# Performance work log

Measured on AMD Instinct MI355X. Metric: run time of the kernel, lower is better.

## Reference

```python
import jax, jax.numpy as jnp
import numpy as np

EPSILON = 0.1


def setup_inputs() -> dict:
    key = jax.random.key(0)
    ks = jax.random.split(key, 6)
    N, E, F_IN, F_OUT, NF = 50000, 800000, 256, 96, 3
    x = jax.random.normal(ks[0], (N, F_IN), dtype=jnp.float32)
    adj_vals = jax.random.uniform(ks[1], (E,), dtype=jnp.float32)
    d_scales = jax.random.uniform(ks[2], (NF, N), dtype=jnp.float32)
    # xavier-uniform-ish weights
    limit = np.sqrt(6.0 / (F_IN + F_OUT)).astype(np.float32)
    weights = jax.random.uniform(ks[3], (NF, F_IN, F_OUT), dtype=jnp.float32,
                                 minval=-limit, maxval=limit)
    bias = jnp.zeros((F_OUT,), dtype=jnp.float32)
    edge_index = jax.random.randint(ks[4], (2, E), 0, N, dtype=jnp.int32)
    return {"x": x, "adj_vals": adj_vals, "d_scales": d_scales,
            "weights": weights, "bias": bias, "edge_index": edge_index}


def reference(x, adj_vals, d_scales, weights, bias, edge_index):
    N = x.shape[0]
    row, col = edge_index[0], edge_index[1]

    # degree with self loops (add_remaining_self_loops adds 1 per node)
    deg = jax.ops.segment_sum(jnp.ones_like(adj_vals), row, num_segments=N) + 1.0
    eps_deg_inv = EPSILON / deg  # [N], diagonal of sparse_degree(..., epsilon)

    def spmm(t):  # symadj @ t via edge list
        return jax.ops.segment_sum(adj_vals[:, None] * t[col], row, num_segments=N)

    out = jnp.zeros((N, weights.shape[2]), dtype=x.dtype)
    n_filters = weights.shape[0]
    for ii in range(n_filters):
        sign = -1.0 if ii == 0 else 1.0  # Ad = symadj -/+ eps*diag(deg^-1)
        t = d_scales[ii][:, None] * (x @ weights[ii])          # D @ (x W)
        t = spmm(t) + sign * eps_deg_inv[:, None] * t          # Ad @ t
        t = d_scales[ii][:, None] * jax.nn.relu(t)             # D @ relu(t)
        out = out + t
    return out + bias
```

## Files before the change

kernel.cpp:

```cpp
#include <hip/hip_runtime.h>

#define EPSILON 0.1f
#define F_IN 256
#define F_OUT 96
#define NF 3
#define TCOLS 288
#define TSTRIDE 320
#define CAP 64
#define BN 96
#define CW 104
#define NCVT (TCOLS * F_IN / 4)

#define RPB 64
#define NBINS 782
#define BCAP 1536
#define EPB 4096

typedef __attribute__((ext_vector_type(8))) short bf8_t;
typedef __attribute__((ext_vector_type(4))) float f32x4;

__device__ inline ushort f2b(float f) {
    union { float f; unsigned u; } v; v.f = f;
    unsigned u = v.u;
    return (ushort)((u + 0x7FFFu + ((u >> 16) & 1u)) >> 16);
}
__device__ inline float blo(unsigned u) { return __uint_as_float(u << 16); }
__device__ inline float bhi(unsigned u) { return __uint_as_float(u & 0xffff0000u); }

__device__ inline bf8_t cvt8(float4 a, float4 b) {
    bf8_t r;
    r[0] = (short)f2b(a.x); r[1] = (short)f2b(a.y);
    r[2] = (short)f2b(a.z); r[3] = (short)f2b(a.w);
    r[4] = (short)f2b(b.x); r[5] = (short)f2b(b.y);
    r[6] = (short)f2b(b.z); r[7] = (short)f2b(b.w);
    return r;
}

__global__ __launch_bounds__(256) void setup_kernel(const float* __restrict__ w,
                                                    ushort* __restrict__ wt,
                                                    int* __restrict__ gcur) {
    int tid = blockIdx.x * 256 + threadIdx.x;
    if (tid < NCVT) {
        int base = tid * 4;
        int gc = base >> 8;
        int k  = base & 255;
        int ii = gc / F_OUT;
        int c  = gc - ii * F_OUT;
        const float* wp = w + (size_t)ii * (F_IN * F_OUT) + (size_t)k * F_OUT + c;
        ushort4 o;
        o.x = f2b(wp[0 * F_OUT]);
        o.y = f2b(wp[1 * F_OUT]);
        o.z = f2b(wp[2 * F_OUT]);
        o.w = f2b(wp[3 * F_OUT]);
        *(ushort4*)(wt + base) = o;
    } else {
        int z = (tid - NCVT) * 4;
        if (z + 3 < NBINS) {
            *(int4*)(gcur + z) = make_int4(0, 0, 0, 0);
        } else {
            for (int j = z; j < NBINS && j >= 0; ++j) gcur[j] = 0;
        }
    }
}

__global__ __launch_bounds__(256) void bin_cvt_kernel(
        const int* __restrict__ row, const int* __restrict__ col,
        const float* __restrict__ vals, int E,
        int* __restrict__ gcur, int2* __restrict__ gout,
        const float* __restrict__ x, ushort* __restrict__ xb, int N, int nbin) {
    __shared__ int2 ord[EPB];
    __shared__ int hist[NBINS];
    __shared__ int gbase[NBINS];
    __shared__ int basex[NBINS];
    __shared__ int ts[512];

    if ((int)blockIdx.x < nbin) {
        int tid = threadIdx.x;
        for (int i = tid; i < NBINS; i += 256) hist[i] = 0;
        __syncthreads();

        int e0 = (int)blockIdx.x * EPB;
        int4 r4[4], c4[4]; float4 v4[4];
        int rank[16], binv[16], valv[16];
        unsigned recx[16];
        #pragma unroll
        for (int g = 0; g < 4; ++g) {
            int e = e0 + tid * 4 + g * 1024;
            if (e + 3 < E) {
                r4[g] = *(const int4*)(row + e);
                c4[g] = *(const int4*)(col + e);
                v4[g] = *(const float4*)(vals + e);
            } else {
                int4 rr, cc; float4 vv;
                int* rp = (int*)&rr; int* cp = (int*)&cc; float* vp = (float*)&vv;
                #pragma unroll
                for (int j = 0; j < 4; ++j) {
                    int ee = e + j;
                    rp[j] = (ee < E) ? row[ee] : -1;
                    cp[j] = (ee < E) ? col[ee] : 0;
                    vp[j] = (ee < E) ? vals[ee] : 0.f;
                }
                r4[g] = rr; c4[g] = cc; v4[g] = vv;
            }
        }
        #pragma unroll
        for (int g = 0; g < 4; ++g) {
            const int* rp = (const int*)&r4[g];
            const int* cp = (const int*)&c4[g];
            const float* vp = (const float*)&v4[g];
            #pragma unroll
            for (int j = 0; j < 4; ++j) {
                int s = g * 4 + j;
                int r = rp[j];
                if (r >= 0) {
                    int b = r >> 6;
                    binv[s] = b;
                    recx[s] = (unsigned)(cp[j] & 0xffff) |
                              ((unsigned)(r & 63) << 16) | ((unsigned)b << 22);
                    valv[s] = __float_as_int(vp[j]);
                    rank[s] = atomicAdd(&hist[b], 1);
                } else {
                    binv[s] = -1; rank[s] = 0; recx[s] = 0; valv[s] = 0;
                }
            }
        }
        __syncthreads();

        int b0 = tid * 4;
        int h0 = (b0     < NBINS) ? hist[b0]     : 0;
        int h1 = (b0 + 1 < NBINS) ? hist[b0 + 1] : 0;
        int h2 = (b0 + 2 < NBINS) ? hist[b0 + 2] : 0;
        int h3 = (b0 + 3 < NBINS) ? hist[b0 + 3] : 0;
        int tot = h0 + h1 + h2 + h3;
        ts[tid] = tot;
        __syncthreads();
        int src = 0;
        #pragma unroll
        for (int off = 1; off < 256; off <<= 1) {
            int v = ts[src * 256 + tid];
            if (tid >= off) v += ts[src * 256 + tid - off];
            ts[(src ^ 1) * 256 + tid] = v;
            __syncthreads();
            src ^= 1;
        }
        int excl = ts[src * 256 + tid] - tot;
        if (b0     < NBINS) basex[b0]     = excl;
        if (b0 + 1 < NBINS) basex[b0 + 1] = excl + h0;
        if (b0 + 2 < NBINS) basex[b0 + 2] = excl + h0 + h1;
        if (b0 + 3 < NBINS) basex[b0 + 3] = excl + h0 + h1 + h2;
        #pragma unroll
        for (int q = 0; q < 4; ++q) {
            int i = b0 + q;
            if (i < NBINS) {
                int h = hist[i];
                gbase[i] = h ? atomicAdd(&gcur[i], h) : 0;
            }
        }
        __syncthreads();

        #pragma unroll
        for (int s = 0; s < 16; ++s)
            if (binv[s] >= 0)
                ord[basex[binv[s]] + rank[s]] = make_int2((int)recx[s], valv[s]);
        __syncthreads();

        int total = ts[src * 256 + 255];
        for (int i = tid; i < total; i += 256) {
            int2 rec = ord[i];
            int b = ((unsigned)rec.x) >> 22;
            int pos = gbase[b] + (i - basex[b]);
            if (pos < BCAP)
                gout[(size_t)b * BCAP + pos] = rec;
        }
    } else {
        size_t base = ((size_t)((int)blockIdx.x - nbin) * 256 + threadIdx.x) * 8;
        if (base < (size_t)N * F_IN) {
            float4 a = *(const float4*)(x + base);
            float4 b = *(const float4*)(x + base + 4);
            bf8_t o = cvt8(a, b);
            *(bf8_t*)(xb + base) = o;
        }
    }
}

__global__ __launch_bounds__(256) void bucket_kernel(
        const int2* __restrict__ gout, const int* __restrict__ gcur,
        int* __restrict__ cnt, int2* __restrict__ evs2, int N) {
    __shared__ int2 buck[RPB * CAP];
    __shared__ int lcnt[RPB];

    int tid = threadIdx.x;
    int b = blockIdx.x;
    if (tid < RPB) lcnt[tid] = 0;
    __syncthreads();

    int nrec = gcur[b];
    if (nrec > BCAP) nrec = BCAP;
    for (int i = tid; i < nrec; i += 256) {
        int2 rec = gout[(size_t)b * BCAP + i];
        int rl = (rec.x >> 16) & 63;
        int c  = rec.x & 0xffff;
        int k = atomicAdd(&lcnt[rl], 1);
        if (k < CAP) buck[rl * CAP + k] = make_int2(c, rec.y);
    }
    __syncthreads();

    int row0 = b * RPB;
    if (tid < RPB && row0 + tid < N) cnt[row0 + tid] = lcnt[tid];

    int lane = tid & 63, wave = tid >> 6;
    for (int r = wave; r < RPB; r += 4) {
        int rowg = row0 + r;
        if (rowg >= N) break;
        int m = min(lcnt[r], CAP);
        if (lane < m)
            evs2[(size_t)rowg * CAP + lane] = buck[r * CAP + lane];
    }
}

__global__ __launch_bounds__(256) void gemm_mfma(const ushort* __restrict__ xb,
                                                 const ushort* __restrict__ wt,
                                                 const float* __restrict__ dsc,
                                                 ushort* __restrict__ t, int N) {
    __shared__ ushort Bs[BN * F_IN];

    int tid = threadIdx.x;
    int lane = tid & 63, wave = tid >> 6;
    int cl = lane & 15, quad = lane >> 4;
    int mb = blockIdx.x / 3, cb = blockIdx.x - mb * 3;
    int gc0 = cb * BN;
    int m0 = mb * 64 + wave * 16;
    int mrow = m0 + cl;
    bool aok = (mrow < N);

    #pragma unroll
    for (int i = 0; i < 12; ++i) {
        int F = tid + i * 256;
        int rem = F & 63;
        int q = rem >> 4, c = rem & 15;
        int ksj = F >> 6;
        int ks = ksj / 6, j = ksj - ks * 6;
        int gc = gc0 + j * 16 + c;
        *(uint4*)(Bs + (size_t)F * 8) =
            *(const uint4*)(wt + (size_t)gc * F_IN + ks * 32 + q * 8);
    }

    uint4 areg[8];
    const ushort* xp = xb + (size_t)mrow * F_IN + quad * 8;
    const uint4 zu = make_uint4(0, 0, 0, 0);
    #pragma unroll
    for (int ks = 0; ks < 8; ++ks)
        areg[ks] = aok ? *(const uint4*)(xp + ks * 32) : zu;

    f32x4 acc[6];
    #pragma unroll
    for (int j = 0; j < 6; ++j) acc[j] = (f32x4){0.f, 0.f, 0.f, 0.f};

    __syncthreads();

    #pragma unroll
    for (int ks = 0; ks < 8; ++ks) {
        bf8_t a = *(const bf8_t*)&areg[ks];
        const ushort* bb = Bs + ((size_t)(ks * 6) * 64 + lane) * 8;
        #pragma unroll
        for (int j = 0; j < 6; ++j) {
            bf8_t b = *(const bf8_t*)(bb + j * 64 * 8);
            acc[j] = __builtin_amdgcn_mfma_f32_16x16x32_bf16(a, b, acc[j], 0, 0, 0);
        }
    }

    __syncthreads();
    ushort* Cw = Bs + wave * (16 * CW);
    float dscv[3][4];
    #pragma unroll
    for (int ii = 0; ii < 3; ++ii)
        #pragma unroll
        for (int r = 0; r < 4; ++r) {
            int rowg = m0 + quad * 4 + r;
            dscv[ii][r] = (rowg < N) ? dsc[(size_t)ii * N + rowg] : 0.f;
        }
    #pragma unroll
    for (int j = 0; j < 6; ++j) {
        int ii = (gc0 + j * 16) / F_OUT;
        #pragma unroll
        for (int r = 0; r < 4; ++r)
            Cw[(quad * 4 + r) * CW + j * 16 + cl] = f2b(dscv[ii][r] * acc[j][r]);
    }
    #pragma unroll
    for (int it = 0; it < 3; ++it) {
        int idx = lane + it * 64;
        int r = idx / 12, ch = idx - r * 12;
        int grow = m0 + r;
        if (grow < N)
            *(uint4*)(t + (size_t)grow * TSTRIDE + gc0 + ch * 8) =
                *(const uint4*)&Cw[r * CW + ch * 8];
    }
}

__device__ inline void acc8(float* acc, uint4 a, float v) {
    acc[0] = fmaf(v, blo(a.x), acc[0]); acc[1] = fmaf(v, bhi(a.x), acc[1]);
    acc[2] = fmaf(v, blo(a.y), acc[2]); acc[3] = fmaf(v, bhi(a.y), acc[3]);
    acc[4] = fmaf(v, blo(a.z), acc[4]); acc[5] = fmaf(v, bhi(a.z), acc[5]);
    acc[6] = fmaf(v, blo(a.w), acc[6]); acc[7] = fmaf(v, bhi(a.w), acc[7]);
}

__global__ __launch_bounds__(256) void spmm_kernel(const ushort* __restrict__ t,
                                                   const int2* __restrict__ evs2,
                                                   const int* __restrict__ cnt,
                                                   const float* __restrict__ dsc,
                                                   const float* __restrict__ bias,
                                                   float* __restrict__ out, int N) {
    int lane = threadIdx.x & 63;
    int wave = threadIdx.x >> 6;
    int n = blockIdx.x * 4 + wave;
    if (n >= N) return;

    int deg = cnt[n];
    int mm = (deg < CAP) ? deg : CAP;
    int s = n * CAP, e = s + mm;
    int coff = (lane < 40) ? lane * 8 : 0;

    float acc[8];
    #pragma unroll
    for (int j = 0; j < 8; ++j) acc[j] = 0.f;

    for (int base = s; base < e; base += 64) {
        int idx = base + lane;
        int2 q = make_int2(0, 0);
        if (idx < e) q = evs2[idx];
        int m = min(64, e - base);
        int j = 0;
        for (; j + 3 < m; j += 4) {
            int c0 = __shfl(q.x, j, 64);
            int c1 = __shfl(q.x, j + 1, 64);
            int c2 = __shfl(q.x, j + 2, 64);
            int c3 = __shfl(q.x, j + 3, 64);
            float v0 = __int_as_float(__shfl(q.y, j, 64));
            float v1 = __int_as_float(__shfl(q.y, j + 1, 64));
            float v2 = __int_as_float(__shfl(q.y, j + 2, 64));
            float v3 = __int_as_float(__shfl(q.y, j + 3, 64));
            uint4 a0 = *(const uint4*)(t + (size_t)c0 * TSTRIDE + coff);
            uint4 a1 = *(const uint4*)(t + (size_t)c1 * TSTRIDE + coff);
            uint4 a2 = *(const uint4*)(t + (size_t)c2 * TSTRIDE + coff);
            uint4 a3 = *(const uint4*)(t + (size_t)c3 * TSTRIDE + coff);
            acc8(acc, a0, v0);
            acc8(acc, a1, v1);
            acc8(acc, a2, v2);
            acc8(acc, a3, v3);
        }
        for (; j < m; ++j) {
            int c = __shfl(q.x, j, 64);
            float v = __int_as_float(__shfl(q.y, j, 64));
            uint4 a = *(const uint4*)(t + (size_t)c * TSTRIDE + coff);
            acc8(acc, a, v);
        }
    }

    float sign = (lane < 12) ? -1.f : 1.f;
    float epsdi = EPSILON / (float)(deg + 1);
    int ii = lane / 12;
    float dscv = (lane < 36) ? dsc[(size_t)ii * N + n] : 0.f;
    uint4 sv = *(const uint4*)(t + (size_t)n * TSTRIDE + coff);
    float se = sign * epsdi;
    float val[8];
    {
        unsigned u;
        u = sv.x; val[0] = fmaf(se, blo(u), acc[0]); val[1] = fmaf(se, bhi(u), acc[1]);
        u = sv.y; val[2] = fmaf(se, blo(u), acc[2]); val[3] = fmaf(se, bhi(u), acc[3]);
        u = sv.z; val[4] = fmaf(se, blo(u), acc[4]); val[5] = fmaf(se, bhi(u), acc[5]);
        u = sv.w; val[6] = fmaf(se, blo(u), acc[6]); val[7] = fmaf(se, bhi(u), acc[7]);
    }
    #pragma unroll
    for (int j = 0; j < 8; ++j) val[j] = fmaxf(val[j], 0.f) * dscv;

    float res[8];
    #pragma unroll
    for (int j = 0; j < 8; ++j) {
        float r1 = __shfl(val[j], lane + 12, 64);
        float r2 = __shfl(val[j], lane + 24, 64);
        res[j] = val[j] + r1 + r2;
    }
    if (lane < 12) {
        float4 b0 = *(const float4*)(bias + lane * 8);
        float4 b1 = *(const float4*)(bias + lane * 8 + 4);
        float4 o0 = make_float4(res[0] + b0.x, res[1] + b0.y, res[2] + b0.z, res[3] + b0.w);
        float4 o1 = make_float4(res[4] + b1.x, res[5] + b1.y, res[6] + b1.z, res[7] + b1.w);
        *(float4*)(out + (size_t)n * F_OUT + lane * 8) = o0;
        *(float4*)(out + (size_t)n * F_OUT + lane * 8 + 4) = o1;
    }
}

extern "C" void kernel_launch(void* const* d_in, const int* in_sizes, int n_in,
                              void* d_out, int out_size, void* d_ws, size_t ws_size,
                              hipStream_t stream) {
    const float* x    = (const float*)d_in[0];
    const float* adj  = (const float*)d_in[1];
    const float* dsc  = (const float*)d_in[2];
    const float* w    = (const float*)d_in[3];
    const float* bias = (const float*)d_in[4];
    const int*   ei   = (const int*)d_in[5];

    int E = in_sizes[1];
    int N = in_sizes[0] / F_IN;
    const int* row = ei;
    const int* col = ei + E;
    float* out = (float*)d_out;

    char* p = (char*)d_ws;
    auto take = [&](size_t bytes) {
        char* r = p;
        p += (bytes + 255) & ~(size_t)255;
        return r;
    };
    int*    cnt  = (int*)take((size_t)N * 4);
    int2*   evs2 = (int2*)take((size_t)N * CAP * 8);
    ushort* wt   = (ushort*)take((size_t)TCOLS * F_IN * 2);
    ushort* xb   = (ushort*)take((size_t)N * F_IN * 2);
    ushort* t    = (ushort*)take(((size_t)N * TSTRIDE + 256) * 2);
    int*    gcur = (int*)take((size_t)NBINS * 4);
    int2*   gout = (int2*)take((size_t)NBINS * BCAP * 8);

    int nzero = (NBINS + 3) / 4;
    setup_kernel<<<(NCVT + nzero + 255) / 256, 256, 0, stream>>>(w, wt, gcur);

    int nbin  = (E + EPB - 1) / EPB;
    int ncvtx = ((N * F_IN / 8) + 255) / 256;
    bin_cvt_kernel<<<nbin + ncvtx, 256, 0, stream>>>(row, col, adj, E, gcur, gout,
                                                     x, xb, N, nbin);
    bucket_kernel<<<NBINS, 256, 0, stream>>>(gout, gcur, cnt, evs2, N);
    gemm_mfma<<<3 * ((N + 63) / 64), 256, 0, stream>>>(xb, wt, dsc, t, N);
    spmm_kernel<<<(N + 3) / 4, 256, 0, stream>>>(t, evs2, cnt, dsc, bias, out, N);
}
```

Baseline: 231.5 us.

## Fuse bucket and GEMM kernels into one launch with XCD-aware tile mapping

```diff
diff --git a/kernel.cpp b/kernel.cpp
--- a/kernel.cpp
+++ b/kernel.cpp
@@ -183,59 +183,64 @@
     }
 }
 
-__global__ __launch_bounds__(256) void bucket_kernel(
+__global__ __launch_bounds__(512) void gemm_bucket(
+        const ushort* __restrict__ xb, const ushort* __restrict__ wt,
+        const float* __restrict__ dsc, ushort* __restrict__ t, int N,
+        int nper, int nw,
         const int2* __restrict__ gout, const int* __restrict__ gcur,
-        int* __restrict__ cnt, int2* __restrict__ evs2, int N) {
-    __shared__ int2 buck[RPB * CAP];
-    __shared__ int lcnt[RPB];
+        int* __restrict__ cnt, int2* __restrict__ evs2) {
+    __shared__ ushort Bs[BN * F_IN];
 
     int tid = threadIdx.x;
-    int b = blockIdx.x;
-    if (tid < RPB) lcnt[tid] = 0;
-    __syncthreads();
-
-    int nrec = gcur[b];
-    if (nrec > BCAP) nrec = BCAP;
-    for (int i = tid; i < nrec; i += 256) {
-        int2 rec = gout[(size_t)b * BCAP + i];
-        int rl = (rec.x >> 16) & 63;
-        int c  = rec.x & 0xffff;
-        int k = atomicAdd(&lcnt[rl], 1);
-        if (k < CAP) buck[rl * CAP + k] = make_int2(c, rec.y);
-    }
-    __syncthreads();
-
-    int row0 = b * RPB;
-    if (tid < RPB && row0 + tid < N) cnt[row0 + tid] = lcnt[tid];
-
-    int lane = tid & 63, wave = tid >> 6;
-    for (int r = wave; r < RPB; r += 4) {
-        int rowg = row0 + r;
-        if (rowg >= N) break;
-        int m = min(lcnt[r], CAP);
-        if (lane < m)
-            evs2[(size_t)rowg * CAP + lane] = buck[r * CAP + lane];
-    }
-}
-
-__global__ __launch_bounds__(256) void gemm_mfma(const ushort* __restrict__ xb,
-                                                 const ushort* __restrict__ wt,
-                                                 const float* __restrict__ dsc,
-                                                 ushort* __restrict__ t, int N) {
-    __shared__ ushort Bs[BN * F_IN];
-
-    int tid = threadIdx.x;
+
+    if ((int)blockIdx.x < NBINS) {
+        int2* buck = (int2*)Bs;
+        int*  lcnt = (int*)(Bs + 16384);
+        int b = blockIdx.x;
+        if (tid < RPB) lcnt[tid] = 0;
+        __syncthreads();
+
+        int nrec = gcur[b];
+        if (nrec > BCAP) nrec = BCAP;
+        for (int i = tid; i < nrec; i += 512) {
+            int2 rec = gout[(size_t)b * BCAP + i];
+            int rl = (rec.x >> 16) & 63;
+            int c  = rec.x & 0xffff;
+            int k = atomicAdd(&lcnt[rl], 1);
+            if (k < CAP) buck[rl * CAP + k] = make_int2(c * TSTRIDE, rec.y);
+        }
+        __syncthreads();
+
+        int row0 = b * RPB;
+        if (tid < RPB && row0 + tid < N) cnt[row0 + tid] = lcnt[tid];
+
+        int lane = tid & 63, wave = tid >> 6;
+        for (int r = wave; r < RPB; r += 8) {
+            int rowg = row0 + r;
+            if (rowg >= N) break;
+            int m = min(lcnt[r], CAP);
+            if (lane < m)
+                evs2[(size_t)rowg * CAP + lane] = buck[r * CAP + lane];
+        }
+        return;
+    }
+
+    int lb = (int)blockIdx.x - NBINS;
+    int xcd = lb & 7, li = lb >> 3;
+    int w = xcd * nper + li;
+    if (w >= nw) return;
+    int mb = w / 3, cb = w - mb * 3;
+
     int lane = tid & 63, wave = tid >> 6;
     int cl = lane & 15, quad = lane >> 4;
-    int mb = blockIdx.x / 3, cb = blockIdx.x - mb * 3;
     int gc0 = cb * BN;
-    int m0 = mb * 64 + wave * 16;
+    int m0 = mb * 128 + wave * 16;
     int mrow = m0 + cl;
     bool aok = (mrow < N);
 
     #pragma unroll
-    for (int i = 0; i < 12; ++i) {
-        int F = tid + i * 256;
+    for (int i = 0; i < 6; ++i) {
+        int F = tid + i * 512;
         int rem = F & 63;
         int q = rem >> 4, c = rem & 15;
         int ksj = F >> 6;
@@ -339,10 +344,10 @@
             float v1 = __int_as_float(__shfl(q.y, j + 1, 64));
             float v2 = __int_as_float(__shfl(q.y, j + 2, 64));
             float v3 = __int_as_float(__shfl(q.y, j + 3, 64));
-            uint4 a0 = *(const uint4*)(t + (size_t)c0 * TSTRIDE + coff);
-            uint4 a1 = *(const uint4*)(t + (size_t)c1 * TSTRIDE + coff);
-            uint4 a2 = *(const uint4*)(t + (size_t)c2 * TSTRIDE + coff);
-            uint4 a3 = *(const uint4*)(t + (size_t)c3 * TSTRIDE + coff);
+            uint4 a0 = *(const uint4*)(t + (size_t)c0 + coff);
+            uint4 a1 = *(const uint4*)(t + (size_t)c1 + coff);
+            uint4 a2 = *(const uint4*)(t + (size_t)c2 + coff);
+            uint4 a3 = *(const uint4*)(t + (size_t)c3 + coff);
             acc8(acc, a0, v0);
             acc8(acc, a1, v1);
             acc8(acc, a2, v2);
@@ -351,7 +356,7 @@
         for (; j < m; ++j) {
             int c = __shfl(q.x, j, 64);
             float v = __int_as_float(__shfl(q.y, j, 64));
-            uint4 a = *(const uint4*)(t + (size_t)c * TSTRIDE + coff);
+            uint4 a = *(const uint4*)(t + (size_t)c + coff);
             acc8(acc, a, v);
         }
     }
@@ -427,7 +432,11 @@
     int ncvtx = ((N * F_IN / 8) + 255) / 256;
     bin_cvt_kernel<<<nbin + ncvtx, 256, 0, stream>>>(row, col, adj, E, gcur, gout,
                                                      x, xb, N, nbin);
-    bucket_kernel<<<NBINS, 256, 0, stream>>>(gout, gcur, cnt, evs2, N);
-    gemm_mfma<<<3 * ((N + 63) / 64), 256, 0, stream>>>(xb, wt, dsc, t, N);
+
+    int nt = (N + 127) / 128;
+    int nw = 3 * nt;
+    int nper = (((nw + 7) / 8) + 2) / 3 * 3;
+    gemm_bucket<<<NBINS + 8 * nper, 512, 0, stream>>>(xb, wt, dsc, t, N, nper, nw,
+                                                      gout, gcur, cnt, evs2);
     spmm_kernel<<<(N + 3) / 4, 256, 0, stream>>>(t, evs2, cnt, dsc, bias, out, N);
 }
```

New measurement: 220.5 us. -4.8%, faster.
